# Kernel optimization log

Measured on AMD Instinct MI355X. Metric: run time of the kernel, lower is better.

Reference implementation:

```python
import jax, jax.numpy as jnp
import numpy as np

B, C, W, H = 16, 512, 32, 32


def spatial_shift1(y):
    # y: [B, W, H, C]; quartile-wise shifts with edge rows/cols left unchanged
    c = y.shape[-1]
    cq = c // 4
    p0 = jnp.concatenate([y[:, :1, :, 0*cq:1*cq], y[:, :-1, :, 0*cq:1*cq]], axis=1)  # w <- w-1
    p1 = jnp.concatenate([y[:, 1:, :, 1*cq:2*cq], y[:, -1:, :, 1*cq:2*cq]], axis=1)  # w <- w+1
    p2 = jnp.concatenate([y[:, :, :1, 2*cq:3*cq], y[:, :, :-1, 2*cq:3*cq]], axis=2)  # h <- h-1
    p3 = jnp.concatenate([y[:, :, 1:, 3*cq:], y[:, :, -1:, 3*cq:]], axis=2)          # h <- h+1
    return jnp.concatenate([p0, p1, p2, p3], axis=-1)


def spatial_shift2(y):
    # same as shift1 with w/h roles swapped
    c = y.shape[-1]
    cq = c // 4
    p0 = jnp.concatenate([y[:, :, :1, 0*cq:1*cq], y[:, :, :-1, 0*cq:1*cq]], axis=2)  # h <- h-1
    p1 = jnp.concatenate([y[:, :, 1:, 1*cq:2*cq], y[:, :, -1:, 1*cq:2*cq]], axis=2)  # h <- h+1
    p2 = jnp.concatenate([y[:, :1, :, 2*cq:3*cq], y[:, :-1, :, 2*cq:3*cq]], axis=1)  # w <- w-1
    p3 = jnp.concatenate([y[:, 1:, :, 3*cq:], y[:, -1:, :, 3*cq:]], axis=1)          # w <- w+1
    return jnp.concatenate([p0, p1, p2, p3], axis=-1)


def setup_inputs() -> dict:
    key = jax.random.key(0)
    ks = jax.random.split(key, 9)
    s = 0.02
    return {
        "x": jax.random.normal(ks[0], (B, C, W, H), dtype=jnp.float32),
        "w1": jax.random.normal(ks[1], (3 * C, C), dtype=jnp.float32) * s,
        "b1": jax.random.normal(ks[2], (3 * C,), dtype=jnp.float32) * s,
        "wa": jax.random.normal(ks[3], (C, C), dtype=jnp.float32) * s,
        "ba": jax.random.normal(ks[4], (C,), dtype=jnp.float32) * s,
        "wb": jax.random.normal(ks[5], (3 * C, C), dtype=jnp.float32) * s,
        "bb": jax.random.normal(ks[6], (3 * C,), dtype=jnp.float32) * s,
        "w2": jax.random.normal(ks[7], (C, C), dtype=jnp.float32) * s,
        "b2": jax.random.normal(ks[8], (C,), dtype=jnp.float32) * s,
    }


def reference(x, w1, b1, wa, ba, wb, bb, w2, b2):
    c = x.shape[1]
    xp = jnp.transpose(x, (0, 2, 3, 1))                     # [B, W, H, C]
    y = jnp.einsum("bwhc,oc->bwho", xp, w1) + b1            # [B, W, H, 3C]
    x1 = spatial_shift1(y[..., :c])
    x2 = spatial_shift2(y[..., c:2 * c])
    x3 = y[..., 2 * c:]
    # SplitAttention: descriptor a = sum over branches and spatial positions
    a = jnp.sum(x1 + x2 + x3, axis=(1, 2))                  # [B, C]
    hat = jax.nn.gelu(a @ wa.T + ba, approximate=False) @ wb.T + bb  # [B, 3C]
    bar = jax.nn.softmax(hat.reshape(-1, 3, c), axis=1)     # softmax over k=3
    g = bar[:, :, None, None, :]                            # [B, 3, 1, 1, C]
    out = g[:, 0] * x1 + g[:, 1] * x2 + g[:, 2] * x3        # [B, W, H, C]
    z = jnp.einsum("bwhc,oc->bwho", out, w2) + b2           # [B, W, H, C]
    return jnp.transpose(z, (0, 3, 1, 2))                   # [B, C, W, H]
```

## Files before the change

kernel.cpp:

```cpp
#include <hip/hip_runtime.h>
#include <stdint.h>

typedef __bf16 bf16x8 __attribute__((ext_vector_type(8)));
typedef float f32x4 __attribute__((ext_vector_type(4)));

#define B_ 16
#define C_ 512
#define S_ 1024
#define N1 1536

__device__ inline unsigned short f2b(float f) {
    unsigned int u = __builtin_bit_cast(unsigned int, f);
    unsigned int lsb = (u >> 16) & 1u;
    u += 0x7fffu + lsb;
    return (unsigned short)(u >> 16);
}
__device__ inline float b2f(unsigned int s) {
    unsigned int u = (s & 0xffffu) << 16;
    return __builtin_bit_cast(float, u);
}

__device__ inline void gl_lds16(const unsigned short* g, unsigned short* l) {
    __builtin_amdgcn_global_load_lds(
        (const __attribute__((address_space(1))) void*)(g),
        (__attribute__((address_space(3))) void*)(l),
        16, 0, 0);
}

__global__ __launch_bounds__(256) void prep_all(
    const float* __restrict__ x, unsigned short* __restrict__ xT,
    const float* __restrict__ w1, const float* __restrict__ w2,
    unsigned short* __restrict__ w1b, unsigned short* __restrict__ w2b,
    float* __restrict__ sums)
{
    int bid = blockIdx.x;
    int t = threadIdx.x;
    if (bid < 8192) {
        __shared__ float tile[32][33];
        int bx = bid & 31;
        int by = (bid >> 5) & 15;
        int bz = bid >> 9;
        int c0 = by * 32;
        int s0 = bx * 32;
        int tx = t & 31, ty = t >> 5;
        const float* xp = x + ((size_t)bz * C_ + c0) * S_ + s0;
#pragma unroll
        for (int i = 0; i < 4; i++)
            tile[ty + i * 8][tx] = xp[(size_t)(ty + i * 8) * S_ + tx];
        __syncthreads();
        unsigned short* op = xT + ((size_t)bz * S_ + s0) * C_ + c0;
#pragma unroll
        for (int i = 0; i < 4; i++)
            op[(size_t)(ty + i * 8) * C_ + tx] = f2b(tile[tx][ty + i * 8]);
    } else {
        int i = (bid - 8192) * 256 + t;
        if (i < 196608) {
            float4 v = ((const float4*)w1)[i];
            ((ushort4*)w1b)[i] = make_ushort4(f2b(v.x), f2b(v.y), f2b(v.z), f2b(v.w));
        } else if (i < 262144) {
            int j = i - 196608;
            float4 v = ((const float4*)w2)[j];
            ((ushort4*)w2b)[j] = make_ushort4(f2b(v.x), f2b(v.y), f2b(v.z), f2b(v.w));
        } else if (i < 292864) {
            int j = i - 262144;
            ((float4*)sums)[j] = make_float4(0.f, 0.f, 0.f, 0.f);
        }
    }
}


__global__ __launch_bounds__(256) void gemm1(
    const unsigned short* __restrict__ A,
    const unsigned short* __restrict__ Wt,
    const float* __restrict__ bias,
    unsigned short* __restrict__ Y,
    float* __restrict__ Tsum, float* __restrict__ H0, float* __restrict__ H31,
    float* __restrict__ C0, float* __restrict__ C31)
{
    const int K = 512;
    const int N = 1536;
    __shared__ __align__(16) unsigned short As[128 * 32];
    __shared__ __align__(16) unsigned short Bs[128 * 32];
    int m0 = blockIdx.x * 128;
    int n0 = blockIdx.y * 128;
    int tid = threadIdx.x;
    int lane = tid & 63, wid = tid >> 6;
    int wm = (wid >> 1) * 64, wn = (wid & 1) * 64;
    int quad = lane >> 4, l16 = lane & 15;
    int ch0 = wid * 128 + lane;
    const unsigned short* Ab = A + (size_t)m0 * K;
    const unsigned short* Bb = Wt + (size_t)n0 * K;

    f32x4 acc[4][4] = {};

    for (int kt = 0; kt < K; kt += 32) {
        __syncthreads();
#pragma unroll
        for (int i = 0; i < 2; i++) {
            int ch = ch0 + i * 64;
            int m = ch >> 2, kc = ch & 3;
            size_t go = (size_t)m * K + kt + kc * 8;
            gl_lds16(Ab + go, &As[ch * 8]);
            gl_lds16(Bb + go, &Bs[ch * 8]);
        }
        __syncthreads();
        bf16x8 af[4], bfr[4];
#pragma unroll
        for (int t = 0; t < 4; t++) {
            af[t]  = *(const bf16x8*)&As[(wm + t * 16 + l16) * 32 + quad * 8];
            bfr[t] = *(const bf16x8*)&Bs[(wn + t * 16 + l16) * 32 + quad * 8];
        }
#pragma unroll
        for (int mt = 0; mt < 4; mt++)
#pragma unroll
            for (int nt = 0; nt < 4; nt++)
                acc[mt][nt] = __builtin_amdgcn_mfma_f32_16x16x32_bf16(af[mt], bfr[nt], acc[mt][nt], 0, 0, 0);
    }

#pragma unroll
    for (int mt = 0; mt < 4; mt++) {
#pragma unroll
        for (int nt = 0; nt < 4; nt++) {
            int n = n0 + wn + nt * 16 + l16;
            float bv = bias[n];
            int mbase = m0 + wm + mt * 16 + quad * 4;
#pragma unroll
            for (int r = 0; r < 4; r++)
                Y[(size_t)(mbase + r) * N + n] = f2b(acc[mt][nt][r] + bv);
        }
    }

    {
        int b = m0 >> 10;
        int wlo = (m0 & 1023) >> 5;
#pragma unroll
        for (int nt = 0; nt < 4; nt++) {
            int n = n0 + wn + nt * 16 + l16;
            float bv = bias[n];
            float tT = 0.f;
#pragma unroll
            for (int mt = 0; mt < 4; mt++)
#pragma unroll
                for (int r = 0; r < 4; r++) tT += acc[mt][nt][r] + bv;
            tT += __shfl_xor(tT, 16);
            tT += __shfl_xor(tT, 32);
            if (quad == 0) {
                atomicAdd(&Tsum[b * 1536 + n], tT);
                float th0 = acc[0][nt][0] + acc[2][nt][0] + 2.f * bv;
                atomicAdd(&H0[b * 1536 + n], th0);
            }
            if (quad == 3) {
                float th31 = acc[1][nt][3] + acc[3][nt][3] + 2.f * bv;
                atomicAdd(&H31[b * 1536 + n], th31);
            }
            if (wlo == 0 && wm == 0) {
                float tc = 0.f;
#pragma unroll
                for (int mt = 0; mt < 2; mt++)
#pragma unroll
                    for (int r = 0; r < 4; r++) tc += acc[mt][nt][r] + bv;
                tc += __shfl_xor(tc, 16);
                tc += __shfl_xor(tc, 32);
                if (quad == 0) atomicAdd(&C0[b * 1536 + n], tc);
            }
            if (wlo == 28 && wm == 64) {
                float tc = 0.f;
#pragma unroll
                for (int mt = 2; mt < 4; mt++)
#pragma unroll
                    for (int r = 0; r < 4; r++) tc += acc[mt][nt][r] + bv;
                tc += __shfl_xor(tc, 16);
                tc += __shfl_xor(tc, 32);
                if (quad == 0) atomicAdd(&C31[b * 1536 + n], tc);
            }
        }
    }
}

__global__ __launch_bounds__(256) void mlp_layer1(
    const float* __restrict__ sums, const float* __restrict__ wa,
    const float* __restrict__ ba, float* __restrict__ h)
{
    __shared__ float sa[512];
    int b = blockIdx.x >> 7;
    int t = threadIdx.x;
    const float* Tp   = sums;
    const float* H0p  = sums + 24576;
    const float* H31p = sums + 49152;
    const float* C0p  = sums + 73728;
    const float* C31p = sums + 98304;
#pragma unroll
    for (int j = 0; j < 2; j++) {
        int c = t + j * 256;
        int q = c >> 7;
        int n1 = b * 1536 + c;
        float t123 = Tp[n1] + Tp[n1 + 512] + Tp[n1 + 1024];
        float sC1 = C0p[n1] - C31p[n1];
        float sH1 = H0p[n1] - H31p[n1];
        float sC2 = C0p[n1 + 512] - C31p[n1 + 512];
        float sH2 = H0p[n1 + 512] - H31p[n1 + 512];
        float e = (q < 2) ? (sC1 + sH2) : (sH1 + sC2);
        sa[c] = t123 + ((q & 1) ? -e : e);
    }
    __syncthreads();
    int lane = t & 63, wid = t >> 6;
    int o = (blockIdx.x & 127) * 4 + wid;
    const float4* wr = (const float4*)(wa + (size_t)o * 512);
    float4 w0 = wr[lane * 2], w1v = wr[lane * 2 + 1];
    float4 a0 = ((const float4*)sa)[lane * 2], a1 = ((const float4*)sa)[lane * 2 + 1];
    float dot = w0.x * a0.x + w0.y * a0.y + w0.z * a0.z + w0.w * a0.w
              + w1v.x * a1.x + w1v.y * a1.y + w1v.z * a1.z + w1v.w * a1.w;
#pragma unroll
    for (int off = 32; off; off >>= 1) dot += __shfl_down(dot, off);
    if (lane == 0) {
        float v = dot + ba[o];
        h[b * 512 + o] = 0.5f * v * (1.0f + erff(v * 0.7071067811865475f));
    }
}

__global__ __launch_bounds__(256) void mlp2_gate(
    const float* __restrict__ h, const float* __restrict__ wb,
    const float* __restrict__ bb, float* __restrict__ g)
{
    __shared__ float hat_s[4][3][16];
    int wv = threadIdx.x >> 6, lane = threadIdx.x & 63;
    int c = blockIdx.x * 4 + wv;
    float4 wr[3][2];
    float bbv[3];
#pragma unroll
    for (int j = 0; j < 3; j++) {
        const float4* p = (const float4*)(wb + (size_t)(j * 512 + c) * 512 + lane * 8);
        wr[j][0] = p[0]; wr[j][1] = p[1];
        bbv[j] = bb[j * 512 + c];
    }
    for (int b = 0; b < 16; b++) {
        const float4* hp = (const float4*)(h + b * 512 + lane * 8);
        float4 h0 = hp[0], h1 = hp[1];
        float d[3];
#pragma unroll
        for (int j = 0; j < 3; j++) {
            d[j] = wr[j][0].x * h0.x + wr[j][0].y * h0.y + wr[j][0].z * h0.z + wr[j][0].w * h0.w
                 + wr[j][1].x * h1.x + wr[j][1].y * h1.y + wr[j][1].z * h1.z + wr[j][1].w * h1.w;
#pragma unroll
            for (int off = 32; off; off >>= 1) d[j] += __shfl_down(d[j], off);
        }
        if (lane == 0) {
#pragma unroll
            for (int j = 0; j < 3; j++) hat_s[wv][j][b] = d[j] + bbv[j];
        }
    }
    __syncthreads();
    if (lane < 16) {
        int b = lane;
        float h0 = hat_s[wv][0][b], h1 = hat_s[wv][1][b], h2 = hat_s[wv][2][b];
        float mx = fmaxf(h0, fmaxf(h1, h2));
        float e0 = __expf(h0 - mx), e1 = __expf(h1 - mx), e2 = __expf(h2 - mx);
        float inv = 1.0f / (e0 + e1 + e2);
        g[(b * 3 + 0) * 512 + c] = e0 * inv;
        g[(b * 3 + 1) * 512 + c] = e1 * inv;
        g[(b * 3 + 2) * 512 + c] = e2 * inv;
    }
}

__global__ __launch_bounds__(256) void combine_g(
    const unsigned short* __restrict__ y, const float* __restrict__ g,
    unsigned short* __restrict__ outT)
{
    int b = blockIdx.y;
    int t = threadIdx.x;
    int w = blockIdx.x * 4 + (t >> 6);
    int c8 = (t & 63) * 8;
    int q = c8 >> 7;
    int dw1 = (q == 0) ? -1 : (q == 1) ? 1 : 0;
    int dh1 = (q == 2) ? -1 : (q == 3) ? 1 : 0;
    int dh2 = (q == 0) ? -1 : (q == 1) ? 1 : 0;
    int dw2 = (q == 2) ? -1 : (q == 3) ? 1 : 0;
    float g0[8], g1[8], g2[8];
    {
        const float4* pa = (const float4*)(g + (b * 3 + 0) * 512 + c8);
        const float4* pb = (const float4*)(g + (b * 3 + 1) * 512 + c8);
        const float4* pc = (const float4*)(g + (b * 3 + 2) * 512 + c8);
        *(float4*)&g0[0] = pa[0]; *(float4*)&g0[4] = pa[1];
        *(float4*)&g1[0] = pb[0]; *(float4*)&g1[4] = pb[1];
        *(float4*)&g2[0] = pc[0]; *(float4*)&g2[4] = pc[1];
    }
    int w1i = min(max(w + dw1, 0), 31);
    int w2i = min(max(w + dw2, 0), 31);
    size_t base = (size_t)b * S_;
    for (int h = 0; h < 32; h++) {
        int h1i = min(max(h + dh1, 0), 31);
        int h2i = min(max(h + dh2, 0), 31);
        uint4 u1 = *(const uint4*)&y[(base + w1i * 32 + h1i) * N1 + c8];
        uint4 u2 = *(const uint4*)&y[(base + w2i * 32 + h2i) * N1 + 512 + c8];
        uint4 u3 = *(const uint4*)&y[(base + w * 32 + h) * N1 + 1024 + c8];
        unsigned int p[4];
        const unsigned int* a1 = &u1.x;
        const unsigned int* a2 = &u2.x;
        const unsigned int* a3 = &u3.x;
#pragma unroll
        for (int k = 0; k < 4; k++) {
            int j = k * 2;
            float lo = g0[j] * b2f(a1[k]) + g1[j] * b2f(a2[k]) + g2[j] * b2f(a3[k]);
            float hi = g0[j + 1] * b2f(a1[k] >> 16) + g1[j + 1] * b2f(a2[k] >> 16) + g2[j + 1] * b2f(a3[k] >> 16);
            p[k] = (unsigned int)f2b(lo) | ((unsigned int)f2b(hi) << 16);
        }
        *(uint4*)&outT[(base + w * 32 + h) * 512 + c8] = make_uint4(p[0], p[1], p[2], p[3]);
    }
}

__global__ __launch_bounds__(256) void gemm2(
    const unsigned short* __restrict__ A,
    const unsigned short* __restrict__ Wt,
    const float* __restrict__ bias,
    float* __restrict__ Z)
{
    const int K = 512;
    __shared__ __align__(16) unsigned short As[128 * 32];
    __shared__ __align__(16) unsigned short Bs[128 * 32];
    int m0 = blockIdx.x * 128;
    int n0 = blockIdx.y * 128;
    int tid = threadIdx.x;
    int lane = tid & 63, wid = tid >> 6;
    int wm = (wid >> 1) * 64, wn = (wid & 1) * 64;
    int quad = lane >> 4, l16 = lane & 15;
    int ch0 = wid * 128 + lane;
    const unsigned short* Ab = A + (size_t)m0 * K;
    const unsigned short* Bb = Wt + (size_t)n0 * K;

    f32x4 acc[4][4] = {};

    for (int kt = 0; kt < K; kt += 32) {
        __syncthreads();
#pragma unroll
        for (int i = 0; i < 2; i++) {
            int ch = ch0 + i * 64;
            int m = ch >> 2, kc = ch & 3;
            size_t go = (size_t)m * K + kt + kc * 8;
            gl_lds16(Ab + go, &As[ch * 8]);
            gl_lds16(Bb + go, &Bs[ch * 8]);
        }
        __syncthreads();
        bf16x8 af[4], bfr[4];
#pragma unroll
        for (int t = 0; t < 4; t++) {
            af[t]  = *(const bf16x8*)&As[(wm + t * 16 + l16) * 32 + quad * 8];
            bfr[t] = *(const bf16x8*)&Bs[(wn + t * 16 + l16) * 32 + quad * 8];
        }
#pragma unroll
        for (int mt = 0; mt < 4; mt++)
#pragma unroll
            for (int nt = 0; nt < 4; nt++)
                acc[mt][nt] = __builtin_amdgcn_mfma_f32_16x16x32_bf16(af[mt], bfr[nt], acc[mt][nt], 0, 0, 0);
    }

#pragma unroll
    for (int mt = 0; mt < 4; mt++) {
#pragma unroll
        for (int nt = 0; nt < 4; nt++) {
            int n = n0 + wn + nt * 16 + l16;
            float bv = bias[n];
            int mbase = m0 + wm + mt * 16 + quad * 4;
            int b = mbase >> 10;
            int s = mbase & 1023;
            float4 v = make_float4(acc[mt][nt][0] + bv, acc[mt][nt][1] + bv,
                                   acc[mt][nt][2] + bv, acc[mt][nt][3] + bv);
            *(float4*)(&Z[((size_t)(b * 512 + n)) * 1024 + s]) = v;
        }
    }
}

extern "C" void kernel_launch(void* const* d_in, const int* in_sizes, int n_in,
                              void* d_out, int out_size, void* d_ws, size_t ws_size,
                              hipStream_t stream) {
    const float* x  = (const float*)d_in[0];
    const float* w1 = (const float*)d_in[1];
    const float* b1 = (const float*)d_in[2];
    const float* wa = (const float*)d_in[3];
    const float* ba = (const float*)d_in[4];
    const float* wb = (const float*)d_in[5];
    const float* bb = (const float*)d_in[6];
    const float* w2 = (const float*)d_in[7];
    const float* b2 = (const float*)d_in[8];
    float* out = (float*)d_out;

    char* ws = (char*)d_ws;
    unsigned short* xT   = (unsigned short*)(ws);
    unsigned short* outT = (unsigned short*)(ws);
    unsigned short* w1b  = (unsigned short*)(ws + 16777216);
    unsigned short* w2b  = (unsigned short*)(ws + 18350080);
    unsigned short* y    = (unsigned short*)(ws + 18874368);
    float* sums          = (float*)(ws + 69206016);
    float* h_buf         = (float*)(ws + 69697536);
    float* g_buf         = (float*)(ws + 69730304);

    float* Tsum = sums;
    float* H0   = sums + 24576;
    float* H31  = sums + 49152;
    float* C0   = sums + 73728;
    float* C31  = sums + 98304;

    prep_all<<<dim3(9336), dim3(256), 0, stream>>>(x, xT, w1, w2, w1b, w2b, sums);
    gemm1<<<dim3(128, 12), dim3(256), 0, stream>>>(
        xT, w1b, b1, y, Tsum, H0, H31, C0, C31);
    mlp_layer1<<<dim3(2048), dim3(256), 0, stream>>>(sums, wa, ba, h_buf);
    mlp2_gate<<<dim3(128), dim3(256), 0, stream>>>(h_buf, wb, bb, g_buf);
    combine_g<<<dim3(8, 16), dim3(256), 0, stream>>>(y, g_buf, outT);
    gemm2<<<dim3(128, 4), dim3(256), 0, stream>>>(outT, w2b, b2, out);
}
```

Baseline: 197.2 us.

## Double-buffer GEMM tiles with register prefetch instead of direct global-to-LDS loads

Both GEMM kernels now prefetch the next K-tile into registers while computing on the current one, and alternate between two LDS buffers. This removes one barrier per iteration and overlaps global-load latency with MFMA work. The cost is twice the LDS footprint, more registers, and dropping the direct global_load_lds path in favour of register staging, which could lower occupancy.

```diff
diff --git a/kernel.cpp b/kernel.cpp
--- a/kernel.cpp
+++ b/kernel.cpp
@@ -18,13 +18,6 @@
 __device__ inline float b2f(unsigned int s) {
     unsigned int u = (s & 0xffffu) << 16;
     return __builtin_bit_cast(float, u);
-}
-
-__device__ inline void gl_lds16(const unsigned short* g, unsigned short* l) {
-    __builtin_amdgcn_global_load_lds(
-        (const __attribute__((address_space(1))) void*)(g),
-        (__attribute__((address_space(3))) void*)(l),
-        16, 0, 0);
 }
 
 __global__ __launch_bounds__(256) void prep_all(
@@ -79,36 +72,49 @@
 {
     const int K = 512;
     const int N = 1536;
-    __shared__ __align__(16) unsigned short As[128 * 32];
-    __shared__ __align__(16) unsigned short Bs[128 * 32];
+    __shared__ __align__(16) unsigned short As[2][128 * 32];
+    __shared__ __align__(16) unsigned short Bs[2][128 * 32];
     int m0 = blockIdx.x * 128;
     int n0 = blockIdx.y * 128;
     int tid = threadIdx.x;
     int lane = tid & 63, wid = tid >> 6;
     int wm = (wid >> 1) * 64, wn = (wid & 1) * 64;
     int quad = lane >> 4, l16 = lane & 15;
-    int ch0 = wid * 128 + lane;
-    const unsigned short* Ab = A + (size_t)m0 * K;
-    const unsigned short* Bb = Wt + (size_t)n0 * K;
+    int ch1 = wid * 128 + lane;
+    int ch2 = ch1 + 64;
+    int lo1 = ch1 * 8, lo2 = ch2 * 8;
+    const unsigned short* pA1 = A + (size_t)m0 * K + (size_t)(ch1 >> 2) * K + (ch1 & 3) * 8;
+    const unsigned short* pA2 = A + (size_t)m0 * K + (size_t)(ch2 >> 2) * K + (ch2 & 3) * 8;
+    const unsigned short* pB1 = Wt + (size_t)n0 * K + (size_t)(ch1 >> 2) * K + (ch1 & 3) * 8;
+    const unsigned short* pB2 = Wt + (size_t)n0 * K + (size_t)(ch2 >> 2) * K + (ch2 & 3) * 8;
 
     f32x4 acc[4][4] = {};
 
-    for (int kt = 0; kt < K; kt += 32) {
+    uint4 ra0 = *(const uint4*)(pA1);
+    uint4 ra1 = *(const uint4*)(pA2);
+    uint4 rb0 = *(const uint4*)(pB1);
+    uint4 rb1 = *(const uint4*)(pB2);
+
+    for (int it = 0; it < 16; it++) {
+        unsigned short* Ac = &As[it & 1][0];
+        unsigned short* Bc = &Bs[it & 1][0];
+        *(uint4*)&Ac[lo1] = ra0;
+        *(uint4*)&Ac[lo2] = ra1;
+        *(uint4*)&Bc[lo1] = rb0;
+        *(uint4*)&Bc[lo2] = rb1;
         __syncthreads();
-#pragma unroll
-        for (int i = 0; i < 2; i++) {
-            int ch = ch0 + i * 64;
-            int m = ch >> 2, kc = ch & 3;
-            size_t go = (size_t)m * K + kt + kc * 8;
-            gl_lds16(Ab + go, &As[ch * 8]);
-            gl_lds16(Bb + go, &Bs[ch * 8]);
-        }
-        __syncthreads();
+        if (it < 15) {
+            int kt = (it + 1) * 32;
+            ra0 = *(const uint4*)(pA1 + kt);
+            ra1 = *(const uint4*)(pA2 + kt);
+            rb0 = *(const uint4*)(pB1 + kt);
+            rb1 = *(const uint4*)(pB2 + kt);
+        }
         bf16x8 af[4], bfr[4];
 #pragma unroll
         for (int t = 0; t < 4; t++) {
-            af[t]  = *(const bf16x8*)&As[(wm + t * 16 + l16) * 32 + quad * 8];
-            bfr[t] = *(const bf16x8*)&Bs[(wn + t * 16 + l16) * 32 + quad * 8];
+            af[t]  = *(const bf16x8*)&Ac[(wm + t * 16 + l16) * 32 + quad * 8];
+            bfr[t] = *(const bf16x8*)&Bc[(wn + t * 16 + l16) * 32 + quad * 8];
         }
 #pragma unroll
         for (int mt = 0; mt < 4; mt++)
@@ -315,36 +321,49 @@
     float* __restrict__ Z)
 {
     const int K = 512;
-    __shared__ __align__(16) unsigned short As[128 * 32];
-    __shared__ __align__(16) unsigned short Bs[128 * 32];
+    __shared__ __align__(16) unsigned short As[2][128 * 32];
+    __shared__ __align__(16) unsigned short Bs[2][128 * 32];
     int m0 = blockIdx.x * 128;
     int n0 = blockIdx.y * 128;
     int tid = threadIdx.x;
     int lane = tid & 63, wid = tid >> 6;
     int wm = (wid >> 1) * 64, wn = (wid & 1) * 64;
     int quad = lane >> 4, l16 = lane & 15;
-    int ch0 = wid * 128 + lane;
-    const unsigned short* Ab = A + (size_t)m0 * K;
-    const unsigned short* Bb = Wt + (size_t)n0 * K;
+    int ch1 = wid * 128 + lane;
+    int ch2 = ch1 + 64;
+    int lo1 = ch1 * 8, lo2 = ch2 * 8;
+    const unsigned short* pA1 = A + (size_t)m0 * K + (size_t)(ch1 >> 2) * K + (ch1 & 3) * 8;
+    const unsigned short* pA2 = A + (size_t)m0 * K + (size_t)(ch2 >> 2) * K + (ch2 & 3) * 8;
+    const unsigned short* pB1 = Wt + (size_t)n0 * K + (size_t)(ch1 >> 2) * K + (ch1 & 3) * 8;
+    const unsigned short* pB2 = Wt + (size_t)n0 * K + (size_t)(ch2 >> 2) * K + (ch2 & 3) * 8;
 
     f32x4 acc[4][4] = {};
 
-    for (int kt = 0; kt < K; kt += 32) {
+    uint4 ra0 = *(const uint4*)(pA1);
+    uint4 ra1 = *(const uint4*)(pA2);
+    uint4 rb0 = *(const uint4*)(pB1);
+    uint4 rb1 = *(const uint4*)(pB2);
+
+    for (int it = 0; it < 16; it++) {
+        unsigned short* Ac = &As[it & 1][0];
+        unsigned short* Bc = &Bs[it & 1][0];
+        *(uint4*)&Ac[lo1] = ra0;
+        *(uint4*)&Ac[lo2] = ra1;
+        *(uint4*)&Bc[lo1] = rb0;
+        *(uint4*)&Bc[lo2] = rb1;
         __syncthreads();
-#pragma unroll
-        for (int i = 0; i < 2; i++) {
-            int ch = ch0 + i * 64;
-            int m = ch >> 2, kc = ch & 3;
-            size_t go = (size_t)m * K + kt + kc * 8;
-            gl_lds16(Ab + go, &As[ch * 8]);
-            gl_lds16(Bb + go, &Bs[ch * 8]);
-        }
-        __syncthreads();
+        if (it < 15) {
+            int kt = (it + 1) * 32;
+            ra0 = *(const uint4*)(pA1 + kt);
+            ra1 = *(const uint4*)(pA2 + kt);
+            rb0 = *(const uint4*)(pB1 + kt);
+            rb1 = *(const uint4*)(pB2 + kt);
+        }
         bf16x8 af[4], bfr[4];
 #pragma unroll
         for (int t = 0; t < 4; t++) {
-            af[t]  = *(const bf16x8*)&As[(wm + t * 16 + l16) * 32 + quad * 8];
-            bfr[t] = *(const bf16x8*)&Bs[(wn + t * 16 + l16) * 32 + quad * 8];
+            af[t]  = *(const bf16x8*)&Ac[(wm + t * 16 + l16) * 32 + quad * 8];
+            bfr[t] = *(const bf16x8*)&Bc[(wn + t * 16 + l16) * 32 + quad * 8];
         }
 #pragma unroll
         for (int mt = 0; mt < 4; mt++)
```

Measured after the change: 194.4 us. About the same (-1.4%).
